# Kernel optimization log

Measured on AMD Instinct MI355X. Metric: run time of the kernel, lower is better.

Reference implementation:

```python
import jax, jax.numpy as jnp
import numpy as np

D_MODEL = 1024
NUM_HEADS = 16
D_HEAD = D_MODEL // NUM_HEADS
B, S = 2, 2048


def setup_inputs() -> dict:
    key = jax.random.key(0)
    ks = jax.random.split(key, 12)
    s = 0.02
    return {
        "query": jax.random.normal(ks[0], (B, S, D_MODEL), jnp.float32),
        "key": jax.random.normal(ks[1], (B, S, D_MODEL), jnp.float32),
        "value": jax.random.normal(ks[2], (B, S, D_MODEL), jnp.float32),
        "mask": jnp.ones((B, 1, 1, S), jnp.float32),
        "W_q": jax.random.normal(ks[3], (D_MODEL, D_MODEL), jnp.float32) * s,
        "b_q": jnp.zeros((D_MODEL,), jnp.float32),
        "W_k": jax.random.normal(ks[4], (D_MODEL, D_MODEL), jnp.float32) * s,
        "b_k": jnp.zeros((D_MODEL,), jnp.float32),
        "W_v": jax.random.normal(ks[5], (D_MODEL, D_MODEL), jnp.float32) * s,
        "b_v": jnp.zeros((D_MODEL,), jnp.float32),
        "W_o": jax.random.normal(ks[6], (D_MODEL, D_MODEL), jnp.float32) * s,
        "b_o": jnp.zeros((D_MODEL,), jnp.float32),
    }


def reference(query, key, value, mask, W_q, b_q, W_k, b_k, W_v, b_v, W_o, b_o):
    # Linear projections (torch nn.Linear: x @ W.T + b; here W stored as [in, out])
    q = query @ W_q + b_q
    k = key @ W_k + b_k
    v = value @ W_v + b_v
    # [B, S, D] -> [B, H, S, Dh]
    def split_heads(x):
        b, s, _ = x.shape
        return x.reshape(b, s, NUM_HEADS, D_HEAD).transpose(0, 2, 1, 3)
    q, k, v = split_heads(q), split_heads(k), split_heads(v)
    # scaled dot-product attention; full [B,H,Sq,Sk] matrix (faithful to source)
    logits = jnp.einsum("bhqd,bhkd->bhqk", q, k) / jnp.sqrt(jnp.float32(D_HEAD))
    logits = logits + (1.0 - mask) * (-1e9)
    attn = jax.nn.softmax(logits, axis=-1)
    # dropout is identity in eval mode
    ctx = jnp.einsum("bhqk,bhkd->bhqd", attn, v)
    ctx = ctx.transpose(0, 2, 1, 3).reshape(ctx.shape[0], -1, D_MODEL)
    out = ctx @ W_o + b_o
    return out, attn
```

## Files before the change

### kernel.cpp

```cpp
#include <hip/hip_runtime.h>
#include <hip/hip_bf16.h>

#define BATCH 2
#define SEQ 2048
#define DM 1024
#define NH 16
#define DH 64
#define MTOT (BATCH*SEQ)

typedef __attribute__((ext_vector_type(8))) short bf16x8;
typedef __attribute__((ext_vector_type(4))) float f32x4;
typedef __attribute__((ext_vector_type(16))) float f32x16;
typedef __attribute__((ext_vector_type(4))) float float4v;
typedef __attribute__((ext_vector_type(8))) unsigned short u16x8;
typedef __attribute__((ext_vector_type(4))) unsigned short u16x4;

#define GLDS16(g, l) __builtin_amdgcn_global_load_lds(                         \
    (const __attribute__((address_space(1))) void*)(g),                        \
    (__attribute__((address_space(3))) void*)(l), 16, 0, 0)

static __device__ __forceinline__ float bf2f(unsigned short u) {
    unsigned int x = ((unsigned int)u) << 16;
    float f; __builtin_memcpy(&f, &x, 4); return f;
}
static __device__ __forceinline__ unsigned short f2bf(float f) {
    unsigned int x; __builtin_memcpy(&x, &f, 4);
    x += 0x7fffu + ((x >> 16) & 1);
    return (unsigned short)(x >> 16);
}
static __device__ __forceinline__ unsigned int cvt_pk_bf16(float a, float b) {
    unsigned int r;
    asm volatile("v_cvt_pk_bf16_f32 %0, %1, %2" : "=v"(r) : "v"(a), "v"(b));
    return r;
}

__global__ __launch_bounds__(256) void prep_kernel(
    const float* __restrict__ q, const float* __restrict__ k, const float* __restrict__ v,
    unsigned short* __restrict__ oq, unsigned short* __restrict__ ok_, unsigned short* __restrict__ ov,
    const float* __restrict__ w0, const float* __restrict__ w1,
    const float* __restrict__ w2, const float* __restrict__ w3,
    unsigned short* __restrict__ t0, unsigned short* __restrict__ t1,
    unsigned short* __restrict__ t2, unsigned short* __restrict__ t3) {
    __shared__ float tile[64][65];
    const int bx = blockIdx.x, t = threadIdx.x;
    if (bx < 6144) {
        const int slab = bx >> 11, bxr = bx & 2047;
        const float* in = slab == 0 ? q : (slab == 1 ? k : v);
        unsigned short* out = slab == 0 ? oq : (slab == 1 ? ok_ : ov);
        size_t i = ((size_t)bxr * 256 + t) * 8;
        float4v a = *(const float4v*)(in + i);
        float4v b = *(const float4v*)(in + i + 4);
        u16x8 r;
        r[0]=f2bf(a[0]); r[1]=f2bf(a[1]); r[2]=f2bf(a[2]); r[3]=f2bf(a[3]);
        r[4]=f2bf(b[0]); r[5]=f2bf(b[1]); r[6]=f2bf(b[2]); r[7]=f2bf(b[3]);
        *(u16x8*)(out + i) = r;
    } else {
        const int i2 = bx - 6144;
        const int z = i2 >> 8, rem = i2 & 255;
        const float* w = z==0 ? w0 : z==1 ? w1 : z==2 ? w2 : w3;
        unsigned short* wt = z==0 ? t0 : z==1 ? t1 : z==2 ? t2 : t3;
        const int k0 = (rem & 15) * 64, n0 = (rem >> 4) * 64;
        const int tr = t >> 4, tc = t & 15;
#pragma unroll
        for (int i = 0; i < 4; ++i) {
            float4v val = *(const float4v*)(w + (size_t)(k0 + tr + 16*i) * DM + n0 + tc*4);
            tile[tr + 16*i][tc*4 + 0] = val[0];
            tile[tr + 16*i][tc*4 + 1] = val[1];
            tile[tr + 16*i][tc*4 + 2] = val[2];
            tile[tr + 16*i][tc*4 + 3] = val[3];
        }
        __syncthreads();
#pragma unroll
        for (int i = 0; i < 4; ++i) {
            u16x4 o;
#pragma unroll
            for (int j = 0; j < 4; ++j) o[j] = f2bf(tile[tc*4 + j][tr + 16*i]);
            *(u16x4*)(wt + (size_t)(n0 + tr + 16*i) * DM + k0 + tc*4) = o;
        }
    }
}

template<int OUTMODE, int BN>
static __device__ __forceinline__ void gemm_body(
    const unsigned short* __restrict__ A, const unsigned short* __restrict__ Bt,
    const float* __restrict__ bias, void* __restrict__ Cout,
    unsigned short* a_lds, unsigned short* b_lds) {
    constexpr int BM = 128, BK = 64, NT = DM / BK, NC = BN / 32;
    const int tid = threadIdx.x;
    const int m0 = blockIdx.y * BM, n0 = blockIdx.x * BN;
    const int w = tid >> 6, l = tid & 63;
    const int lr = l & 15, lg = l >> 4;
    const int wm = (w >> 1) * 64, wn = (w & 1) * (BN/2);
    f32x4 acc[4][NC] = {};

    auto stage = [&](int buf, int kt) {
        const int k0 = kt * BK;
#pragma unroll
        for (int i = 0; i < 4; ++i) {
            int u = i*256 + tid;
            int row = u >> 3, slot = u & 7;
            int sc = (slot ^ (row & 7)) * 8;
            GLDS16(A + (size_t)(m0 + row)*DM + k0 + sc, a_lds + buf*BM*BK + u*8);
        }
#pragma unroll
        for (int i = 0; i < NC; ++i) {
            int u = i*256 + tid;
            int row = u >> 3, slot = u & 7;
            int sc = (slot ^ (row & 7)) * 8;
            GLDS16(Bt + (size_t)(n0 + row)*DM + k0 + sc, b_lds + buf*BN*BK + u*8);
        }
    };

    stage(0, 0);
    for (int kt = 0; kt < NT; ++kt) {
        __syncthreads();
        if (kt < NT-1) stage((kt+1)&1, kt+1);
        const char* ab = (const char*)(a_lds + (kt&1)*BM*BK);
        const char* bb = (const char*)(b_lds + (kt&1)*BN*BK);
        bf16x8 af[4][2], bfr[NC][2];
#pragma unroll
        for (int r = 0; r < 4; ++r)
#pragma unroll
            for (int kc = 0; kc < 2; ++kc) {
                int row = wm + r*16 + lr;
                af[r][kc] = *(const bf16x8*)(ab + row*128 + ((kc*64 + lg*16) ^ ((row&7)<<4)));
            }
#pragma unroll
        for (int c = 0; c < NC; ++c)
#pragma unroll
            for (int kc = 0; kc < 2; ++kc) {
                int row = wn + c*16 + lr;
                bfr[c][kc] = *(const bf16x8*)(bb + row*128 + ((kc*64 + lg*16) ^ ((row&7)<<4)));
            }
#pragma unroll
        for (int r = 0; r < 4; ++r)
#pragma unroll
            for (int c = 0; c < NC; ++c)
#pragma unroll
                for (int kc = 0; kc < 2; ++kc)
                    acc[r][c] = __builtin_amdgcn_mfma_f32_16x16x32_bf16(af[r][kc], bfr[c][kc], acc[r][c], 0, 0, 0);
    }

#pragma unroll
    for (int r = 0; r < 4; ++r)
#pragma unroll
        for (int c = 0; c < NC; ++c) {
            int m = m0 + wm + r*16 + lg*4;
            int n = n0 + wn + c*16 + lr;
            float bb = bias[n];
            if constexpr (OUTMODE == 1) {
                float* o = (float*)Cout;
#pragma unroll
                for (int j = 0; j < 4; ++j) o[(size_t)(m+j)*DM + n] = acc[r][c][j] + bb;
            } else if constexpr (OUTMODE == 0) {
                unsigned short* o = (unsigned short*)Cout;
#pragma unroll
                for (int j = 0; j < 4; ++j) o[(size_t)(m+j)*DM + n] = f2bf(acc[r][c][j] + bb);
            } else {
                unsigned short* o = (unsigned short*)Cout;
                int bb_ = m >> 11, kk = m & (SEQ-1);
                int bh = bb_ * NH + (n >> 6), d = n & 63;
                u16x4 ov;
#pragma unroll
                for (int j = 0; j < 4; ++j) ov[j] = f2bf(acc[r][c][j] + bb);
                *(u16x4*)(o + ((size_t)bh*DH + d)*SEQ + kk) = ov;
            }
        }
}

__global__ __launch_bounds__(256) void gemm_qkv_kernel(
    const unsigned short* __restrict__ A0, const unsigned short* __restrict__ A1, const unsigned short* __restrict__ A2,
    const unsigned short* __restrict__ B0, const unsigned short* __restrict__ B1, const unsigned short* __restrict__ B2,
    const float* __restrict__ c0, const float* __restrict__ c1, const float* __restrict__ c2,
    unsigned short* __restrict__ O0, unsigned short* __restrict__ O1, unsigned short* __restrict__ O2) {
    __shared__ __align__(16) unsigned short smem[2*128*64 + 2*128*64];
    const int z = blockIdx.z;
    const unsigned short* A = z==0 ? A0 : z==1 ? A1 : A2;
    const unsigned short* B = z==0 ? B0 : z==1 ? B1 : B2;
    const float* c = z==0 ? c0 : z==1 ? c1 : c2;
    unsigned short* O = z==0 ? O0 : z==1 ? O1 : O2;
    if (z == 2) gemm_body<2, 128>(A, B, c, O, smem, smem + 2*128*64);
    else        gemm_body<0, 128>(A, B, c, O, smem, smem + 2*128*64);
}

__global__ __launch_bounds__(256, 3) void gemm_out_kernel(
    const unsigned short* __restrict__ A, const unsigned short* __restrict__ Bt,
    const float* __restrict__ bias, float* __restrict__ Cout) {
    __shared__ __align__(16) unsigned short smem[2*128*64 + 2*64*64];
    gemm_body<1, 64>(A, Bt, bias, Cout, smem, smem + 2*128*64);
}

__global__ __launch_bounds__(512, 4) void attn_kernel(
    const unsigned short* __restrict__ qw, const unsigned short* __restrict__ kw,
    const unsigned short* __restrict__ vtg, const float* __restrict__ mask,
    float* __restrict__ attn_out, unsigned short* __restrict__ ctx) {
    constexpr int QB = 128, KB = 64, NT2 = SEQ / KB / 2;
    __shared__ __align__(16) unsigned short smem[2*2*KB*DH + 2*2*KB*DH];
    unsigned short* kbuf = smem;
    unsigned short* vbuf = smem + 4*KB*DH;
    const int tid = threadIdx.x, w = tid >> 6, l = tid & 63;
    const int hh = w >> 2, ws = w & 3;
    const int q32 = l & 31, hi = l >> 5;
    const int u0 = (blockIdx.x & 7) * 64 + (blockIdx.x >> 3);
    const int qblk = u0 & 15, bh = u0 >> 4;
    const int b = bh >> 4, h = bh & 15;
    const int q0 = qblk * QB;
    const int q = q0 + ws*32 + q32;
    const int kbase = hh * (SEQ/2);

    bf16x8 qf[4];
    {
        const unsigned short* qp = qw + ((size_t)(b*SEQ + q))*DM + h*DH + hi*8;
#pragma unroll
        for (int ks = 0; ks < 4; ++ks) {
            bf16x8 t = *(const bf16x8*)(qp + ks*16);
#pragma unroll
            for (int j = 0; j < 8; ++j) t[j] = (short)f2bf(bf2f((unsigned short)t[j]) * 0.125f);
            qf[ks] = t;
        }
    }

    auto stageK = [&](int buf, int kt) {
#pragma unroll
        for (int hf = 0; hf < 2; ++hf) {
            int row = tid >> 3, slot = tid & 7;
            int sc = (slot ^ (row & 7)) * 8;
            const unsigned short* base = kw + ((size_t)(b*SEQ + hf*(SEQ/2) + kt*KB + row))*DM + h*DH;
            GLDS16(base + sc, kbuf + (buf*2 + hf)*KB*DH + tid*8);
        }
    };
    auto stageV = [&](int buf, int kt) {
#pragma unroll
        for (int hf = 0; hf < 2; ++hf) {
            int row = tid >> 3, slot = tid & 7;
            int sc = (slot ^ (row & 7)) * 8;
            const unsigned short* base = vtg + ((size_t)bh*DH + row)*SEQ + hf*(SEQ/2) + kt*KB;
            GLDS16(base + sc, vbuf + (buf*2 + hf)*KB*DH + tid*8);
        }
    };

    const float* mrow = mask + (size_t)b*SEQ + kbase;

    float rs = 0.f;
    stageK(0, 0);
    for (int kt = 0; kt < NT2; ++kt) {
        __syncthreads();
        if (kt < NT2-1) stageK((kt+1)&1, kt+1);
        const char* kb = (const char*)(kbuf + ((kt&1)*2 + hh)*KB*DH);
#pragma unroll
        for (int sub = 0; sub < 2; ++sub) {
            f32x16 s = {};
#pragma unroll
            for (int ks = 0; ks < 4; ++ks) {
                int key = sub*32 + q32;
                bf16x8 kf = *(const bf16x8*)(kb + key*128 + ((ks*32 + hi*16) ^ ((key&7)<<4)));
                s = __builtin_amdgcn_mfma_f32_32x32x16_bf16(kf, qf[ks], s, 0, 0, 0);
            }
#pragma unroll
            for (int rq = 0; rq < 4; ++rq) {
                float4v m4 = *(const float4v*)(mrow + kt*KB + sub*32 + rq*8 + hi*4);
#pragma unroll
                for (int r = 0; r < 4; ++r)
                    rs += __expf(s[rq*4 + r] + (1.0f - m4[r]) * (-1e9f));
            }
        }
    }
    rs += __shfl_xor(rs, 32);
    {
        float* rbuf = (float*)smem;
        __syncthreads();
        rbuf[w*64 + l] = rs;
        __syncthreads();
        rs += rbuf[(w ^ 4)*64 + l];
        __syncthreads();
    }
    const float rinv = 1.0f / rs;

    f32x16 oacc[2] = {};
    float* attn_row = attn_out + ((size_t)bh*SEQ + q)*SEQ + kbase;
    stageK(0, 0); stageV(0, 0);
    for (int kt = 0; kt < NT2; ++kt) {
        __syncthreads();
        if (kt < NT2-1) { stageK((kt+1)&1, kt+1); stageV((kt+1)&1, kt+1); }
        const char* kb = (const char*)(kbuf + ((kt&1)*2 + hh)*KB*DH);
        const char* vb = (const char*)(vbuf + ((kt&1)*2 + hh)*KB*DH);
#pragma unroll
        for (int sub = 0; sub < 2; ++sub) {
            f32x16 s = {};
#pragma unroll
            for (int ks = 0; ks < 4; ++ks) {
                int key = sub*32 + q32;
                bf16x8 kf = *(const bf16x8*)(kb + key*128 + ((ks*32 + hi*16) ^ ((key&7)<<4)));
                s = __builtin_amdgcn_mfma_f32_32x32x16_bf16(kf, qf[ks], s, 0, 0, 0);
            }
            float p[16];
#pragma unroll
            for (int rq = 0; rq < 4; ++rq) {
                float4v m4 = *(const float4v*)(mrow + kt*KB + sub*32 + rq*8 + hi*4);
                float4v pv;
#pragma unroll
                for (int r = 0; r < 4; ++r) {
                    pv[r] = __expf(s[rq*4 + r] + (1.0f - m4[r]) * (-1e9f)) * rinv;
                    p[rq*4 + r] = pv[r];
                }
                *(float4v*)(attn_row + kt*KB + sub*32 + rq*8 + hi*4) = pv;
            }
#pragma unroll
            for (int half = 0; half < 2; ++half) {
                unsigned int w0 = cvt_pk_bf16(p[half*8+0], p[half*8+1]);
                unsigned int w1 = cvt_pk_bf16(p[half*8+2], p[half*8+3]);
                unsigned int w2 = cvt_pk_bf16(p[half*8+4], p[half*8+5]);
                unsigned int w3 = cvt_pk_bf16(p[half*8+6], p[half*8+7]);
                asm volatile("v_permlane32_swap_b32 %0, %1" : "+v"(w0), "+v"(w2));
                asm volatile("v_permlane32_swap_b32 %0, %1" : "+v"(w1), "+v"(w3));
                union { unsigned int uu[4]; bf16x8 v; } pa;
                pa.uu[0] = w0; pa.uu[1] = w1; pa.uu[2] = w2; pa.uu[3] = w3;
                const int ks4 = sub*2 + half;
#pragma unroll
                for (int dsub = 0; dsub < 2; ++dsub) {
                    int d = dsub*32 + q32;
                    bf16x8 vf = *(const bf16x8*)(vb + d*128 + ((ks4*32 + hi*16) ^ ((d&7)<<4)));
                    oacc[dsub] = __builtin_amdgcn_mfma_f32_32x32x16_bf16(pa.v, vf, oacc[dsub], 0, 0, 0);
                }
            }
        }
    }

    float* cbuf = (float*)smem;
    __syncthreads();
    if (w >= 4) {
        int base = ((w - 4)*64 + l) * 36;
        *(f32x16*)(cbuf + base) = oacc[0];
        *(f32x16*)(cbuf + base + 16) = oacc[1];
    }
    __syncthreads();
    if (w < 4) {
        int base = (w*64 + l) * 36;
        oacc[0] += *(const f32x16*)(cbuf + base);
        oacc[1] += *(const f32x16*)(cbuf + base + 16);
#pragma unroll
        for (int dsub = 0; dsub < 2; ++dsub) {
            int d = h*DH + dsub*32 + q32;
#pragma unroll
            for (int reg = 0; reg < 16; ++reg) {
                int qr = q0 + ws*32 + (reg&3) + 8*(reg>>2) + 4*hi;
                ctx[(size_t)(b*SEQ + qr)*DM + d] = f2bf(oacc[dsub][reg]);
            }
        }
    }
}

extern "C" void kernel_launch(void* const* d_in, const int* in_sizes, int n_in,
                              void* d_out, int out_size, void* d_ws, size_t ws_size,
                              hipStream_t stream) {
    const float* query = (const float*)d_in[0];
    const float* key_  = (const float*)d_in[1];
    const float* value = (const float*)d_in[2];
    const float* mask  = (const float*)d_in[3];
    const float* W_q = (const float*)d_in[4];
    const float* b_q = (const float*)d_in[5];
    const float* W_k = (const float*)d_in[6];
    const float* b_k = (const float*)d_in[7];
    const float* W_v = (const float*)d_in[8];
    const float* b_v = (const float*)d_in[9];
    const float* W_o = (const float*)d_in[10];
    const float* b_o = (const float*)d_in[11];

    char* ws = (char*)d_ws;
    const size_t SZ = (size_t)MTOT * DM * 2;
    unsigned short* xq  = (unsigned short*)(ws);
    unsigned short* xk  = (unsigned short*)(ws + SZ);
    unsigned short* xv  = (unsigned short*)(ws + 2*SZ);
    unsigned short* wtq = (unsigned short*)(ws + 3*SZ);
    unsigned short* wtk = wtq + (size_t)DM*DM;
    unsigned short* wtv = wtk + (size_t)DM*DM;
    unsigned short* wto = wtv + (size_t)DM*DM;
    unsigned short* qws = (unsigned short*)(ws + 4*SZ);
    unsigned short* kws = (unsigned short*)(ws + 5*SZ);
    unsigned short* vtg = (unsigned short*)(ws + 6*SZ);
    unsigned short* ctx = (unsigned short*)(ws + 7*SZ);
    float* out_f  = (float*)d_out;
    float* attn_f = out_f + (size_t)MTOT * DM;

    prep_kernel<<<dim3(7168), 256, 0, stream>>>(query, key_, value, xq, xk, xv,
                                                W_q, W_k, W_v, W_o, wtq, wtk, wtv, wto);
    gemm_qkv_kernel<<<dim3(8, 32, 3), 256, 0, stream>>>(xq, xk, xv, wtq, wtk, wtv,
                                                        b_q, b_k, b_v, qws, kws, vtg);
    attn_kernel<<<dim3(512), 512, 0, stream>>>(qws, kws, vtg, mask, attn_f, ctx);
    gemm_out_kernel<<<dim3(16, 32), 256, 0, stream>>>(ctx, wto, b_o, out_f);
}
```

Before: 287.4 us.

## Relax attention barrier waits, precompute mask in LDS, prioritize MFMA waves

In the second attention pass, the full __syncthreads is replaced by an explicit s_waitcnt vmcnt(8) plus s_barrier. This keeps the previous iteration's attention-probability global stores in flight while still waiting for the staged K/V loads. The additive mask term is computed once per block into extra LDS, which removes the per-element global mask loads and arithmetic. MFMA sections are wrapped in s_setprio, and the exp/store/convert work is interleaved per half. The relaxed wait relies on the exact number of outstanding vector memory operations, and the added LDS could limit occupancy.

```diff
diff --git a/kernel.cpp b/kernel.cpp
--- a/kernel.cpp
+++ b/kernel.cpp
@@ -195,9 +195,10 @@
     const unsigned short* __restrict__ vtg, const float* __restrict__ mask,
     float* __restrict__ attn_out, unsigned short* __restrict__ ctx) {
     constexpr int QB = 128, KB = 64, NT2 = SEQ / KB / 2;
-    __shared__ __align__(16) unsigned short smem[2*2*KB*DH + 2*2*KB*DH];
+    __shared__ __align__(16) unsigned short smem[4*KB*DH + 4*KB*DH + 4096];
     unsigned short* kbuf = smem;
     unsigned short* vbuf = smem + 4*KB*DH;
+    float* madd_f = (float*)(smem + 8*KB*DH);
     const int tid = threadIdx.x, w = tid >> 6, l = tid & 63;
     const int hh = w >> 2, ws = w & 3;
     const int q32 = l & 31, hi = l >> 5;
@@ -208,6 +209,15 @@
     const int q = q0 + ws*32 + q32;
     const int kbase = hh * (SEQ/2);
 
+    {
+        int idx = tid * 4;
+        float4v m4 = *(const float4v*)(mask + (size_t)b*SEQ + idx);
+        float4v md;
+#pragma unroll
+        for (int r = 0; r < 4; ++r) md[r] = (1.0f - m4[r]) * (-1e9f);
+        *(float4v*)(madd_f + idx) = md;
+    }
+
     bf16x8 qf[4];
     {
         const unsigned short* qp = qw + ((size_t)(b*SEQ + q))*DM + h*DH + hi*8;
@@ -239,8 +249,6 @@
         }
     };
 
-    const float* mrow = mask + (size_t)b*SEQ + kbase;
-
     float rs = 0.f;
     stageK(0, 0);
     for (int kt = 0; kt < NT2; ++kt) {
@@ -250,18 +258,20 @@
 #pragma unroll
         for (int sub = 0; sub < 2; ++sub) {
             f32x16 s = {};
+            __builtin_amdgcn_s_setprio(1);
 #pragma unroll
             for (int ks = 0; ks < 4; ++ks) {
                 int key = sub*32 + q32;
                 bf16x8 kf = *(const bf16x8*)(kb + key*128 + ((ks*32 + hi*16) ^ ((key&7)<<4)));
                 s = __builtin_amdgcn_mfma_f32_32x32x16_bf16(kf, qf[ks], s, 0, 0, 0);
             }
+            __builtin_amdgcn_s_setprio(0);
 #pragma unroll
             for (int rq = 0; rq < 4; ++rq) {
-                float4v m4 = *(const float4v*)(mrow + kt*KB + sub*32 + rq*8 + hi*4);
+                float4v m4 = *(const float4v*)(madd_f + kbase + kt*KB + sub*32 + rq*8 + hi*4);
 #pragma unroll
                 for (int r = 0; r < 4; ++r)
-                    rs += __expf(s[rq*4 + r] + (1.0f - m4[r]) * (-1e9f));
+                    rs += __expf(s[rq*4 + r] + m4[r]);
             }
         }
     }
@@ -280,48 +290,58 @@
     float* attn_row = attn_out + ((size_t)bh*SEQ + q)*SEQ + kbase;
     stageK(0, 0); stageV(0, 0);
     for (int kt = 0; kt < NT2; ++kt) {
-        __syncthreads();
+        if (kt == 0) { asm volatile("s_waitcnt vmcnt(0)" ::: "memory"); }
+        else         { asm volatile("s_waitcnt vmcnt(8)" ::: "memory"); }
+        __builtin_amdgcn_s_barrier();
+        __builtin_amdgcn_sched_barrier(0);
         if (kt < NT2-1) { stageK((kt+1)&1, kt+1); stageV((kt+1)&1, kt+1); }
         const char* kb = (const char*)(kbuf + ((kt&1)*2 + hh)*KB*DH);
         const char* vb = (const char*)(vbuf + ((kt&1)*2 + hh)*KB*DH);
 #pragma unroll
         for (int sub = 0; sub < 2; ++sub) {
             f32x16 s = {};
+            __builtin_amdgcn_s_setprio(1);
 #pragma unroll
             for (int ks = 0; ks < 4; ++ks) {
                 int key = sub*32 + q32;
                 bf16x8 kf = *(const bf16x8*)(kb + key*128 + ((ks*32 + hi*16) ^ ((key&7)<<4)));
                 s = __builtin_amdgcn_mfma_f32_32x32x16_bf16(kf, qf[ks], s, 0, 0, 0);
             }
-            float p[16];
-#pragma unroll
-            for (int rq = 0; rq < 4; ++rq) {
-                float4v m4 = *(const float4v*)(mrow + kt*KB + sub*32 + rq*8 + hi*4);
-                float4v pv;
-#pragma unroll
-                for (int r = 0; r < 4; ++r) {
-                    pv[r] = __expf(s[rq*4 + r] + (1.0f - m4[r]) * (-1e9f)) * rinv;
-                    p[rq*4 + r] = pv[r];
+            __builtin_amdgcn_s_setprio(0);
+#pragma unroll
+            for (int half = 0; half < 2; ++half) {
+                float4v pv0, pv1;
+                {
+                    const int rq = half*2;
+                    float4v m4 = *(const float4v*)(madd_f + kbase + kt*KB + sub*32 + rq*8 + hi*4);
+#pragma unroll
+                    for (int r = 0; r < 4; ++r) pv0[r] = __expf(s[rq*4 + r] + m4[r]) * rinv;
+                    *(float4v*)(attn_row + kt*KB + sub*32 + rq*8 + hi*4) = pv0;
                 }
-                *(float4v*)(attn_row + kt*KB + sub*32 + rq*8 + hi*4) = pv;
-            }
-#pragma unroll
-            for (int half = 0; half < 2; ++half) {
-                unsigned int w0 = cvt_pk_bf16(p[half*8+0], p[half*8+1]);
-                unsigned int w1 = cvt_pk_bf16(p[half*8+2], p[half*8+3]);
-                unsigned int w2 = cvt_pk_bf16(p[half*8+4], p[half*8+5]);
-                unsigned int w3 = cvt_pk_bf16(p[half*8+6], p[half*8+7]);
+                {
+                    const int rq = half*2 + 1;
+                    float4v m4 = *(const float4v*)(madd_f + kbase + kt*KB + sub*32 + rq*8 + hi*4);
+#pragma unroll
+                    for (int r = 0; r < 4; ++r) pv1[r] = __expf(s[rq*4 + r] + m4[r]) * rinv;
+                    *(float4v*)(attn_row + kt*KB + sub*32 + rq*8 + hi*4) = pv1;
+                }
+                unsigned int w0 = cvt_pk_bf16(pv0[0], pv0[1]);
+                unsigned int w1 = cvt_pk_bf16(pv0[2], pv0[3]);
+                unsigned int w2 = cvt_pk_bf16(pv1[0], pv1[1]);
+                unsigned int w3 = cvt_pk_bf16(pv1[2], pv1[3]);
                 asm volatile("v_permlane32_swap_b32 %0, %1" : "+v"(w0), "+v"(w2));
                 asm volatile("v_permlane32_swap_b32 %0, %1" : "+v"(w1), "+v"(w3));
                 union { unsigned int uu[4]; bf16x8 v; } pa;
                 pa.uu[0] = w0; pa.uu[1] = w1; pa.uu[2] = w2; pa.uu[3] = w3;
                 const int ks4 = sub*2 + half;
+                __builtin_amdgcn_s_setprio(1);
 #pragma unroll
                 for (int dsub = 0; dsub < 2; ++dsub) {
                     int d = dsub*32 + q32;
                     bf16x8 vf = *(const bf16x8*)(vb + d*128 + ((ks4*32 + hi*16) ^ ((d&7)<<4)));
                     oacc[dsub] = __builtin_amdgcn_mfma_f32_32x32x16_bf16(pa.v, vf, oacc[dsub], 0, 0, 0);
                 }
+                __builtin_amdgcn_s_setprio(0);
             }
         }
     }
```

New measurement: 292.4 us. No clear change (+1.7%).
